# Kernel tuning notes

Hardware: AMD Instinct MI355X
Metric: run time of the kernel (lower is better)

Reference implementation:

```python
import jax, jax.numpy as jnp
import numpy as np

B, S, H = 256, 4096, 64

def setup_inputs() -> dict:
    key = jax.random.key(0)
    ks = jax.random.split(key, 6)
    x = jax.random.normal(ks[0], (B, S), dtype=jnp.float32)
    # e = nn.Linear(1, H)
    W_e = jax.random.normal(ks[1], (H, 1), dtype=jnp.float32)
    b_e = jax.random.normal(ks[2], (H,), dtype=jnp.float32) * 0.01
    # PhaseAccumulator learnable per-unit frequency
    omega = 1.0 + 0.1 * jax.random.normal(ks[3], (H,), dtype=jnp.float32)
    # r = nn.Linear(3*H, 1)
    W_r = jax.random.normal(ks[4], (1, 3 * H), dtype=jnp.float32) * (1.0 / np.sqrt(3 * H))
    b_r = jnp.zeros((1,), dtype=jnp.float32)
    return {"x": x, "W_e": W_e, "b_e": b_e, "omega": omega, "W_r": W_r, "b_r": b_r}

def reference(x, W_e, b_e, omega, W_r, b_r):
    # per-step 1->H linear, vectorized over all timesteps: p[b,s,h]
    p = x[:, :, None] * W_e[:, 0] + b_e                 # [B,S,H]
    # xp = stack([cos p, sin p]); accumulator delta = atan2(sin p, cos p) = wrap(p)
    delta = jnp.arctan2(jnp.sin(p), jnp.cos(p))         # [B,S,H], wrapped to (-pi, pi]
    # ph_t = ph_{t-1} + omega * delta_t, ph_0 = 0  ->  cumulative sum over time
    Hseq = jnp.cumsum(omega * delta, axis=1)            # [B,S,H] all phase states
    ph = Hseq[:, -1]                                    # [B,H] final phase
    feat = jnp.concatenate([jnp.cos(ph), jnp.sin(ph), ph], axis=1)  # [B,3H]
    out = feat @ W_r.T + b_r                            # [B,1]
    return out, Hseq
```

## Files before the change

kernel.cpp:

```cpp
#include <hip/hip_runtime.h>

#define B_SZ   256
#define S_SZ   4096
#define H_SZ   64
#define NCHUNK 16
#define CHUNK  (S_SZ / NCHUNK)

__device__ __forceinline__ float wrap_delta(float p) {
    const float INV2PI   = 0.15915494309189535f;
    const float TWOPI_HI = 6.2831854820251465f;
    const float TWOPI_LO = -1.7484556000744887e-7f;
    float n = rintf(p * INV2PI);
    float d = fmaf(n, -TWOPI_HI, p);
    d = fmaf(n, -TWOPI_LO, d);
    return d;
}

__global__ __launch_bounds__(256) void k_partials(
    const float* __restrict__ x, const float* __restrict__ W_e,
    const float* __restrict__ b_e, float* __restrict__ ws)
{
    int tid   = blockIdx.x * 256 + threadIdx.x;
    int wid   = tid >> 6;
    int lane  = threadIdx.x & 63;
    int b     = wid >> 4;
    int chunk = wid & (NCHUNK - 1);

    float we = W_e[lane];
    float be = b_e[lane];

    const float* xp = x + b * S_SZ + chunk * CHUNK;
    float acc = 0.f;
    for (int r = 0; r < CHUNK / 64; ++r) {
        float xv = xp[r * 64 + lane];
        #pragma unroll
        for (int j = 0; j < 64; ++j) {
            float xs = __shfl(xv, j, 64);
            float p  = fmaf(xs, we, be);
            acc += wrap_delta(p);
        }
    }
    ws[wid * 64 + lane] = acc;
}

__global__ __launch_bounds__(256) void k_scan(
    const float* __restrict__ x, const float* __restrict__ W_e,
    const float* __restrict__ b_e, const float* __restrict__ omega,
    const float* __restrict__ W_r, const float* __restrict__ b_r,
    const float* __restrict__ ws, float* __restrict__ out,
    float* __restrict__ hseq)
{
    int tid   = blockIdx.x * 256 + threadIdx.x;
    int wid   = tid >> 6;
    int lane  = threadIdx.x & 63;
    int b     = wid >> 4;
    int chunk = wid & (NCHUNK - 1);

    float we = W_e[lane];
    float be = b_e[lane];
    float om = omega[lane];

    float base = 0.f;
    for (int c = 0; c < chunk; ++c)
        base += ws[(b * NCHUNK + c) * 64 + lane];
    float obase = om * base;

    const float* xp = x + b * S_SZ + chunk * CHUNK;
    float* hp = hseq + ((size_t)(b * S_SZ + chunk * CHUNK)) * H_SZ + lane;

    float acc = 0.f;
    float Hval = 0.f;
    for (int r = 0; r < CHUNK / 64; ++r) {
        float xv = xp[r * 64 + lane];
        #pragma unroll
        for (int j = 0; j < 64; ++j) {
            float xs = __shfl(xv, j, 64);
            float p  = fmaf(xs, we, be);
            acc += wrap_delta(p);
            Hval = fmaf(om, acc, obase);
            __builtin_nontemporal_store(Hval, hp);
            hp += H_SZ;
        }
    }

    if (chunk == NCHUNK - 1) {
        float ph = Hval;
        float v = cosf(ph) * W_r[lane]
                + sinf(ph) * W_r[H_SZ + lane]
                + ph       * W_r[2 * H_SZ + lane];
        #pragma unroll
        for (int off = 32; off > 0; off >>= 1)
            v += __shfl_down(v, off, 64);
        if (lane == 0) out[b] = v + b_r[0];
    }
}

extern "C" void kernel_launch(void* const* d_in, const int* in_sizes, int n_in,
                              void* d_out, int out_size, void* d_ws, size_t ws_size,
                              hipStream_t stream) {
    const float* x     = (const float*)d_in[0];
    const float* W_e   = (const float*)d_in[1];
    const float* b_e   = (const float*)d_in[2];
    const float* omega = (const float*)d_in[3];
    const float* W_r   = (const float*)d_in[4];
    const float* b_r   = (const float*)d_in[5];

    float* out  = (float*)d_out;
    float* hseq = out + B_SZ;
    float* ws   = (float*)d_ws;

    dim3 blk(256);
    dim3 grid(B_SZ * NCHUNK / 4);

    k_partials<<<grid, blk, 0, stream>>>(x, W_e, b_e, ws);
    k_scan<<<grid, blk, 0, stream>>>(x, W_e, b_e, omega, W_r, b_r, ws, out, hseq);
}
```

Baseline: 295.6 us.

## Use scalar loads, algebraic partial sums, and more chunks for phase scan

The partials kernel now sums the rounding counts and the raw x values separately, then rebuilds the wrapped-delta sum with a single closing FMA instead of wrapping every step. Both kernels read x through a wave-uniform pointer so the loads can become scalar loads, replacing the per-step cross-lane shuffles. NCHUNK doubles to 32 to expose more waves, and launch bounds add an occupancy hint. The reassociated summation changes float rounding slightly, and more chunks lengthen the serial base-prefix loop in the scan kernel.

```diff
diff --git a/kernel.cpp b/kernel.cpp
--- a/kernel.cpp
+++ b/kernel.cpp
@@ -3,47 +3,50 @@
 #define B_SZ   256
 #define S_SZ   4096
 #define H_SZ   64
-#define NCHUNK 16
+#define NCHUNK 32
 #define CHUNK  (S_SZ / NCHUNK)
 
-__device__ __forceinline__ float wrap_delta(float p) {
-    const float INV2PI   = 0.15915494309189535f;
-    const float TWOPI_HI = 6.2831854820251465f;
-    const float TWOPI_LO = -1.7484556000744887e-7f;
-    float n = rintf(p * INV2PI);
-    float d = fmaf(n, -TWOPI_HI, p);
-    d = fmaf(n, -TWOPI_LO, d);
-    return d;
+#define INV2PI   0.15915494309189535f
+#define TWOPI_HI 6.2831854820251465f
+#define TWOPI_LO (-1.7484556000744887e-7f)
+
+__device__ __forceinline__ const float* uniform_ptr(const float* p) {
+    uint64_t u = (uint64_t)(uintptr_t)p;
+    uint32_t lo = __builtin_amdgcn_readfirstlane((uint32_t)u);
+    uint32_t hi = __builtin_amdgcn_readfirstlane((uint32_t)(u >> 32));
+    return (const float*)(uintptr_t)(((uint64_t)hi << 32) | lo);
 }
 
-__global__ __launch_bounds__(256) void k_partials(
+__global__ __launch_bounds__(256, 4) void k_partials(
     const float* __restrict__ x, const float* __restrict__ W_e,
     const float* __restrict__ b_e, float* __restrict__ ws)
 {
     int tid   = blockIdx.x * 256 + threadIdx.x;
     int wid   = tid >> 6;
     int lane  = threadIdx.x & 63;
-    int b     = wid >> 4;
+    int b     = wid >> 5;
     int chunk = wid & (NCHUNK - 1);
 
     float we = W_e[lane];
     float be = b_e[lane];
 
-    const float* xp = x + b * S_SZ + chunk * CHUNK;
-    float acc = 0.f;
-    for (int r = 0; r < CHUNK / 64; ++r) {
-        float xv = xp[r * 64 + lane];
-        #pragma unroll
-        for (int j = 0; j < 64; ++j) {
-            float xs = __shfl(xv, j, 64);
-            float p  = fmaf(xs, we, be);
-            acc += wrap_delta(p);
-        }
+    const float* xpu = uniform_ptr(x + b * S_SZ + chunk * CHUNK);
+    float accN = 0.f;
+    float accX = 0.f;
+    #pragma unroll 16
+    for (int j = 0; j < CHUNK; ++j) {
+        float xs = xpu[j];
+        float p  = fmaf(xs, we, be);
+        accN += rintf(p * INV2PI);
+        accX += xs;
     }
-    ws[wid * 64 + lane] = acc;
+    float sP = fmaf(we, accX, (float)CHUNK * be);
+    float d  = fmaf(accN, -TWOPI_HI, sP);
+    d        = fmaf(accN, -TWOPI_LO, d);
+    ws[wid * 64 + lane] = d;
 }
 
-__global__ __launch_bounds__(256) void k_scan(
+__global__ __launch_bounds__(256, 4) void k_scan(
     const float* __restrict__ x, const float* __restrict__ W_e,
     const float* __restrict__ b_e, const float* __restrict__ omega,
     const float* __restrict__ W_r, const float* __restrict__ b_r,
@@ -53,7 +56,7 @@
     int tid   = blockIdx.x * 256 + threadIdx.x;
     int wid   = tid >> 6;
     int lane  = threadIdx.x & 63;
-    int b     = wid >> 4;
+    int b     = wid >> 5;
     int chunk = wid & (NCHUNK - 1);
 
     float we = W_e[lane];
@@ -65,22 +68,21 @@
         base += ws[(b * NCHUNK + c) * 64 + lane];
     float obase = om * base;
 
-    const float* xp = x + b * S_SZ + chunk * CHUNK;
-    float* hp = hseq + ((size_t)(b * S_SZ + chunk * CHUNK)) * H_SZ + lane;
+    const float* xpu = uniform_ptr(x + b * S_SZ + chunk * CHUNK);
+    float* hp = hseq + (size_t)(b * S_SZ + chunk * CHUNK) * H_SZ + lane;
 
-    float acc = 0.f;
-    float Hval = 0.f;
-    for (int r = 0; r < CHUNK / 64; ++r) {
-        float xv = xp[r * 64 + lane];
-        #pragma unroll
-        for (int j = 0; j < 64; ++j) {
-            float xs = __shfl(xv, j, 64);
-            float p  = fmaf(xs, we, be);
-            acc += wrap_delta(p);
-            Hval = fmaf(om, acc, obase);
-            __builtin_nontemporal_store(Hval, hp);
-            hp += H_SZ;
-        }
+    float acc  = 0.f;
+    float Hval = obase;
+    #pragma unroll 16
+    for (int j = 0; j < CHUNK; ++j) {
+        float xs = xpu[j];
+        float p  = fmaf(xs, we, be);
+        float n  = rintf(p * INV2PI);
+        float d0 = fmaf(n, -TWOPI_HI, p);
+        d0       = fmaf(n, -TWOPI_LO, d0);
+        acc += d0;
+        Hval = fmaf(om, acc, obase);
+        __builtin_nontemporal_store(Hval, hp + (size_t)j * H_SZ);
     }
 
     if (chunk == NCHUNK - 1) {
```

After: 294.8 us. No clear change (-0.3%).
